# Performance work log

Hardware: AMD Instinct MI355X
Metric: run time of the kernel (lower is better)

The kernel has to match this reference:

```python
import jax, jax.numpy as jnp
import numpy as np

N = 12288
D = 128
NUM_BATCH = 32
EPS = 1e-8


def setup_inputs() -> dict:
    key = jax.random.key(0)
    kq, kk, kv, kb = jax.random.split(key, 4)
    Q = jax.random.normal(kq, (N, D), dtype=jnp.float32)
    K = jax.random.normal(kk, (N, D), dtype=jnp.float32)
    V = jax.random.normal(kv, (N, D), dtype=jnp.float32)
    batch_seg = jnp.sort(jax.random.randint(kb, (N,), 0, NUM_BATCH, dtype=jnp.int32))
    return {"Q": Q, "K": K, "V": V, "num_batch": NUM_BATCH, "batch_seg": batch_seg}


def reference(Q, K, V, num_batch, batch_seg):
    d = Q.shape[-1]
    dot = Q @ K.T                                   # [N, N]
    # NOTE: faithful to original: subtract GLOBAL max, then divide by sqrt(d)
    A = jnp.exp((dot - jnp.max(dot)) / jnp.sqrt(jnp.float32(d)))
    if num_batch > 1:
        mask = (batch_seg[None, :] == batch_seg[:, None])  # block-diagonal
        A = jnp.where(mask, A, jnp.zeros((), A.dtype))
    norm = jnp.sum(A, axis=-1, keepdims=True) + EPS
    A_weights = A / norm
    return A_weights @ V
```

## Files before the change

### kernel.cpp

```cpp
#include <hip/hip_runtime.h>


#define NN 12288
#define DD 128
#define NB 32
#define PS_LD 40
#define VTS 12424

typedef __attribute__((ext_vector_type(8))) short short8;
typedef __attribute__((ext_vector_type(4))) float float4v;

__device__ __forceinline__ short f2bf(float f) {
  unsigned u = __builtin_bit_cast(unsigned, f);
  return (short)((u + 0x7FFFu + ((u >> 16) & 1u)) >> 16);
}

__device__ __forceinline__ float bf2f(short s) {
  return __builtin_bit_cast(float, ((unsigned)(unsigned short)s) << 16);
}

__device__ __forceinline__ short8 ld8_bf16(const float* p) {
  float4v f0 = *(const float4v*)p;
  float4v f1 = *(const float4v*)(p + 4);
  short8 s;
  s[0] = f2bf(f0[0]); s[1] = f2bf(f0[1]); s[2] = f2bf(f0[2]); s[3] = f2bf(f0[3]);
  s[4] = f2bf(f1[0]); s[5] = f2bf(f1[1]); s[6] = f2bf(f1[2]); s[7] = f2bf(f1[3]);
  return s;
}

__device__ __forceinline__ void dma16(const short* gsrc, short* ldst) {
  auto g = (const __attribute__((address_space(1))) void*)(unsigned long long)gsrc;
  auto l = (__attribute__((address_space(3))) void*)(unsigned)(unsigned long long)ldst;
  __builtin_amdgcn_global_load_lds(g, l, 16, 0, 0);
}

__global__ __launch_bounds__(256) void prep_kernel(
    const float* __restrict__ K, const float* __restrict__ V,
    const int* __restrict__ seg,
    short* __restrict__ Kb, short* __restrict__ Vtb, int* __restrict__ starts) {
  const int tid = threadIdx.x;
  const int b = blockIdx.x;
  if (b < 768) {
    const size_t base = (size_t)b * 2048 + (size_t)tid * 8;
    *(short8*)(Kb + base) = ld8_bf16(K + base);
  } else if (b < 864) {
    __shared__ __align__(16) short Ts[DD * 136];
    const int kt = (b - 768) * 128;
#pragma unroll
    for (int rep = 0; rep < 16; ++rep) {
      int v = rep * 256 + tid;
      int key = v >> 5, c4 = (v & 31) * 4;
      float4v f = *(const float4v*)(V + (size_t)(kt + key) * DD + c4);
      Ts[(c4 + 0) * 136 + key] = f2bf(f[0]);
      Ts[(c4 + 1) * 136 + key] = f2bf(f[1]);
      Ts[(c4 + 2) * 136 + key] = f2bf(f[2]);
      Ts[(c4 + 3) * 136 + key] = f2bf(f[3]);
    }
    __syncthreads();
    const int c16 = (tid & 15) * 8;
#pragma unroll
    for (int rep = 0; rep < 8; ++rep) {
      int d = rep * 16 + (tid >> 4);
      short8 s = *(const short8*)&Ts[d * 136 + c16];
      *(short8*)(Vtb + (size_t)d * VTS + kt + c16) = s;
    }
  } else {
    int i = (b - 864) * 256 + tid;
    int s = seg[i];
    int sp = (i == 0) ? -1 : seg[i - 1];
    for (int bb = sp + 1; bb <= s; ++bb) starts[bb] = i;
    if (i == NN - 1)
      for (int bb = s + 1; bb <= NB; ++bb) starts[bb] = NN;
  }
}

__device__ __forceinline__ void issue_tile(
    const short* __restrict__ Kb, const short* __restrict__ Vtb,
    short* KshP, short* VshP, int j0, int wave, int lane) {
#pragma unroll
  for (int i = 0; i < 2; ++i) {
    const int R = wave * 8 + i * 4;
    const int row = R + (lane >> 4);
    const int dchunk = (lane & 15) ^ (row & 15);
    dma16(Kb + (size_t)(j0 + row) * DD + dchunk * 8, KshP + R * 128);
  }
#pragma unroll
  for (int i = 0; i < 2; ++i) {
    const int D = wave * 32 + i * 16;
    const int dr = D + (lane >> 2);
    const int vchunk = (lane & 3) ^ ((lane >> 2) & 3);
    dma16(Vtb + (size_t)dr * VTS + j0 + vchunk * 8, VshP + D * 32);
  }
}

__global__ __launch_bounds__(256, 4) void attn_kernel(
    const float* __restrict__ Q, const short* __restrict__ Kb,
    const short* __restrict__ Vtb, const int* __restrict__ seg,
    const int* __restrict__ starts,
    short* __restrict__ Op, float* __restrict__ lp) {
  __shared__ __align__(16) short Ksh[2][32 * 128];
  __shared__ __align__(16) short Vsh[2][128 * 32];
  __shared__ __align__(16) short Ps[4][16 * PS_LD];

  const int tid = threadIdx.x;
  const int wave = tid >> 6;
  const int lane = tid & 63;
  const int c = lane & 15;
  const int quad = lane >> 4;

  const int bid = blockIdx.x;
  const int y = bid >> 3;
  const int rg = (bid & 7) * 24 + (y >> 2);
  const int sk = y & 3;
  const int i0 = rg * 64;
  const int i0w = i0 + wave * 16;

  const int L = starts[seg[i0]];
  const int H = starts[seg[i0 + 63] + 1];
  const int Lm = L & ~31;
  const int nck = (H - Lm + 31) >> 5;
  const int ck0 = (nck * sk) >> 2;
  const int ck1 = (nck * (sk + 1)) >> 2;
  const int nt = ck1 - ck0;

  int st_r[4], en_r[4];
#pragma unroll
  for (int r = 0; r < 4; ++r) {
    int s = seg[i0w + quad * 4 + r];
    st_r[r] = starts[s];
    en_r[r] = starts[s + 1];
  }

  short8 qf[4];
  {
    const float* qrow = Q + (size_t)(i0w + c) * DD + quad * 8;
#pragma unroll
    for (int kc = 0; kc < 4; ++kc) qf[kc] = ld8_bf16(qrow + kc * 32);
  }

  float4v acc[8];
#pragma unroll
  for (int n = 0; n < 8; ++n) acc[n] = (float4v){0.f, 0.f, 0.f, 0.f};
  float l_part[4] = {0.f, 0.f, 0.f, 0.f};

  const float scale = 0.08838834764831845f;

  if (nt > 0)
    issue_tile(Kb, Vtb, &Ksh[0][0], &Vsh[0][0], Lm + ck0 * 32, wave, lane);
  __syncthreads();

  for (int t = 0; t < nt; ++t) {
    const int j0 = Lm + (ck0 + t) * 32;
    const int p = t & 1;
    if (t + 1 < nt)
      issue_tile(Kb, Vtb, &Ksh[p ^ 1][0], &Vsh[p ^ 1][0], j0 + 32, wave, lane);

    float4v s0 = (float4v){0.f, 0.f, 0.f, 0.f};
    float4v s1 = (float4v){0.f, 0.f, 0.f, 0.f};
    const short* Kp = &Ksh[p][0];
#pragma unroll
    for (int kc = 0; kc < 4; ++kc) {
      const int pos = ((kc * 4 + quad) ^ c) * 8;
      short8 b0 = *(const short8*)(Kp + c * 128 + pos);
      short8 b1 = *(const short8*)(Kp + (16 + c) * 128 + pos);
      s0 = __builtin_amdgcn_mfma_f32_16x16x32_bf16(qf[kc], b0, s0, 0, 0, 0);
      s1 = __builtin_amdgcn_mfma_f32_16x16x32_bf16(qf[kc], b1, s1, 0, 0, 0);
    }

    const int ja = j0 + c, jb = ja + 16;
    short* prow = &Ps[wave][0];
#pragma unroll
    for (int r = 0; r < 4; ++r) {
      float pa = (ja >= st_r[r] && ja < en_r[r]) ? __expf(s0[r] * scale) : 0.f;
      float pb = (jb >= st_r[r] && jb < en_r[r]) ? __expf(s1[r] * scale) : 0.f;
      l_part[r] += pa + pb;
      int row = quad * 4 + r;
      prow[row * PS_LD + c]      = f2bf(pa);
      prow[row * PS_LD + 16 + c] = f2bf(pb);
    }
    short8 pf = *(const short8*)&Ps[wave][c * PS_LD + quad * 8];

    const short* Vp = &Vsh[p][0];
    const int vpos = (quad ^ (c & 3)) * 8;
#pragma unroll
    for (int n = 0; n < 8; ++n) {
      short8 vf = *(const short8*)(Vp + (n * 16 + c) * 32 + vpos);
      acc[n] = __builtin_amdgcn_mfma_f32_16x16x32_bf16(pf, vf, acc[n], 0, 0, 0);
    }

    __syncthreads();
  }

  float lrow[4];
#pragma unroll
  for (int r = 0; r < 4; ++r) {
    float l = l_part[r];
    l += __shfl_xor(l, 1, 64);
    l += __shfl_xor(l, 2, 64);
    l += __shfl_xor(l, 4, 64);
    l += __shfl_xor(l, 8, 64);
    lrow[r] = l;
  }

  short* OpW = Op + ((size_t)sk * NN + i0w) * DD;
#pragma unroll
  for (int n = 0; n < 8; ++n)
#pragma unroll
    for (int r = 0; r < 4; ++r)
      OpW[(quad * 4 + r) * DD + n * 16 + c] = f2bf(acc[n][r]);
  if (c == 0) {
#pragma unroll
    for (int r = 0; r < 4; ++r) lp[sk * NN + i0w + quad * 4 + r] = lrow[r];
  }
}

__global__ __launch_bounds__(256) void combine_kernel(
    const short* __restrict__ Op, const float* __restrict__ lp,
    float* __restrict__ out) {
  const int u = blockIdx.x * 256 + threadIdx.x;
  const int row = u >> 4, c8 = (u & 15) * 8;
  float l = lp[row] + lp[NN + row] + lp[2 * NN + row] + lp[3 * NN + row];
  float o[8] = {0.f, 0.f, 0.f, 0.f, 0.f, 0.f, 0.f, 0.f};
#pragma unroll
  for (int s = 0; s < 4; ++s) {
    short8 t = *(const short8*)(Op + ((size_t)s * NN + row) * DD + c8);
#pragma unroll
    for (int j = 0; j < 8; ++j) o[j] += bf2f(t[j]);
  }
  const float inv = 1.f / (l + 1e-8f);
  float4v o0 = (float4v){o[0] * inv, o[1] * inv, o[2] * inv, o[3] * inv};
  float4v o1 = (float4v){o[4] * inv, o[5] * inv, o[6] * inv, o[7] * inv};
  *(float4v*)(out + (size_t)row * DD + c8)     = o0;
  *(float4v*)(out + (size_t)row * DD + c8 + 4) = o1;
}

#define KT_LD 136
#define VT_LD 40
typedef __attribute__((ext_vector_type(4))) short short4v;

__global__ __launch_bounds__(256) void attn_fallback(
    const float* __restrict__ Q, const float* __restrict__ K,
    const float* __restrict__ V, const int* __restrict__ seg,
    float* __restrict__ out) {
  __shared__ __align__(16) short Kt[32 * KT_LD];
  __shared__ __align__(16) short Vt[DD * VT_LD];
  __shared__ __align__(16) short Ps[4][16 * PS_LD];
  const int tid = threadIdx.x, wave = tid >> 6, lane = tid & 63;
  const int c = lane & 15, quad = lane >> 4;
  const int m0 = blockIdx.x * 64, i0 = m0 + wave * 16;
  const int segFirst = seg[m0], segLast = seg[m0 + 63];
  int lo = 0, hb = NN;
  while (lo < hb) { int mid = (lo + hb) >> 1; if (seg[mid] < segFirst) lo = mid + 1; else hb = mid; }
  int hi = lo, hb2 = NN;
  while (hi < hb2) { int mid = (hi + hb2) >> 1; if (seg[mid] <= segLast) hi = mid + 1; else hb2 = mid; }
  short8 qf[4];
  const float* qrow = Q + (size_t)(i0 + c) * DD + quad * 8;
#pragma unroll
  for (int kc = 0; kc < 4; ++kc) qf[kc] = ld8_bf16(qrow + kc * 32);
  int seg_r[4];
#pragma unroll
  for (int r = 0; r < 4; ++r) seg_r[r] = seg[i0 + quad * 4 + r];
  float4v acc[8];
#pragma unroll
  for (int n = 0; n < 8; ++n) acc[n] = (float4v){0.f, 0.f, 0.f, 0.f};
  float l_part[4] = {0.f, 0.f, 0.f, 0.f};
  const float scale = 0.08838834764831845f;
  for (int j0 = lo; j0 < hi; j0 += 32) {
    __syncthreads();
    {
      int row = tid >> 3, ch = tid & 7;
      int jj = j0 + row; if (jj > NN - 1) jj = NN - 1;
      const float* kp = K + (size_t)jj * DD + ch * 16;
      short* dst = &Kt[row * KT_LD + ch * 16];
#pragma unroll
      for (int q4 = 0; q4 < 4; ++q4) {
        float4v f = *(const float4v*)(kp + q4 * 4);
        short4v s;
        s[0] = f2bf(f[0]); s[1] = f2bf(f[1]); s[2] = f2bf(f[2]); s[3] = f2bf(f[3]);
        *(short4v*)(dst + q4 * 4) = s;
      }
    }
    {
      int d = tid & 127, jh = tid >> 7;
      float vv[16];
#pragma unroll
      for (int j = 0; j < 16; ++j) {
        int jj = j0 + jh * 16 + j; if (jj > NN - 1) jj = NN - 1;
        vv[j] = V[(size_t)jj * DD + d];
      }
      short8 a, b2;
#pragma unroll
      for (int j = 0; j < 8; ++j) { a[j] = f2bf(vv[j]); b2[j] = f2bf(vv[8 + j]); }
      *(short8*)&Vt[d * VT_LD + jh * 16] = a;
      *(short8*)&Vt[d * VT_LD + jh * 16 + 8] = b2;
    }
    __syncthreads();
    float4v s0 = (float4v){0.f, 0.f, 0.f, 0.f};
    float4v s1 = (float4v){0.f, 0.f, 0.f, 0.f};
    const short* krow0 = &Kt[c * KT_LD + quad * 8];
    const short* krow1 = &Kt[(16 + c) * KT_LD + quad * 8];
#pragma unroll
    for (int kc = 0; kc < 4; ++kc) {
      short8 b0 = *(const short8*)(krow0 + kc * 32);
      short8 b1 = *(const short8*)(krow1 + kc * 32);
      s0 = __builtin_amdgcn_mfma_f32_16x16x32_bf16(qf[kc], b0, s0, 0, 0, 0);
      s1 = __builtin_amdgcn_mfma_f32_16x16x32_bf16(qf[kc], b1, s1, 0, 0, 0);
    }
    int ja = j0 + c, jb = ja + 16;
    int sa = seg[ja < NN ? ja : NN - 1];
    int sb = seg[jb < NN ? jb : NN - 1];
    bool va = ja < hi, vb = jb < hi;
    short* prow = &Ps[wave][0];
#pragma unroll
    for (int r = 0; r < 4; ++r) {
      float pa = (va && sa == seg_r[r]) ? __expf(s0[r] * scale) : 0.f;
      float pb = (vb && sb == seg_r[r]) ? __expf(s1[r] * scale) : 0.f;
      l_part[r] += pa + pb;
      int row = quad * 4 + r;
      prow[row * PS_LD + c] = f2bf(pa);
      prow[row * PS_LD + 16 + c] = f2bf(pb);
    }
    short8 pf = *(const short8*)&Ps[wave][c * PS_LD + quad * 8];
#pragma unroll
    for (int n = 0; n < 8; ++n) {
      short8 vfr = *(const short8*)&Vt[(n * 16 + c) * VT_LD + quad * 8];
      acc[n] = __builtin_amdgcn_mfma_f32_16x16x32_bf16(pf, vfr, acc[n], 0, 0, 0);
    }
  }
  float linv[4];
#pragma unroll
  for (int r = 0; r < 4; ++r) {
    float l = l_part[r];
    l += __shfl_xor(l, 1, 64);
    l += __shfl_xor(l, 2, 64);
    l += __shfl_xor(l, 4, 64);
    l += __shfl_xor(l, 8, 64);
    linv[r] = 1.f / (l + 1e-8f);
  }
#pragma unroll
  for (int n = 0; n < 8; ++n)
#pragma unroll
    for (int r = 0; r < 4; ++r)
      out[(size_t)(i0 + quad * 4 + r) * DD + n * 16 + c] = acc[n][r] * linv[r];
}

extern "C" void kernel_launch(void* const* d_in, const int* in_sizes, int n_in,
                              void* d_out, int out_size, void* d_ws, size_t ws_size,
                              hipStream_t stream) {
  const float* Q = (const float*)d_in[0];
  const float* K = (const float*)d_in[1];
  const float* V = (const float*)d_in[2];
  const int* seg = (const int*)d_in[4];
  float* out = (float*)d_out;

  const size_t kb_bytes = (size_t)NN * DD * sizeof(short);
  const size_t vt_bytes = (size_t)DD * VTS * sizeof(short);
  const size_t st_bytes = 64 * sizeof(int);
  const size_t op_bytes = (size_t)4 * NN * DD * sizeof(short);
  const size_t lp_bytes = (size_t)4 * NN * sizeof(float);
  const size_t need = kb_bytes + vt_bytes + st_bytes + op_bytes + lp_bytes;

  if (ws_size >= need) {
    char* w = (char*)d_ws;
    short* Kb  = (short*)w;                     w += kb_bytes;
    short* Vtb = (short*)w;                     w += vt_bytes;
    int* starts = (int*)w;                      w += st_bytes;
    short* Op = (short*)w;                      w += op_bytes;
    float* lp = (float*)w;
    prep_kernel<<<864 + NN / 256, 256, 0, stream>>>(K, V, seg, Kb, Vtb, starts);
    attn_kernel<<<768, 256, 0, stream>>>(Q, Kb, Vtb, seg, starts, Op, lp);
    combine_kernel<<<768, 256, 0, stream>>>(Op, lp, out);
  } else {
    attn_fallback<<<NN / 64, 256, 0, stream>>>(Q, K, V, seg, out);
  }
}
```

Measured before the change: 95.59 us.

## Fuse split-K combine into attention kernel and pre-swizzle V into tile-blocked layout

Drops the separate combine kernel and the bf16 partial-output buffers. The attention kernel now uses 512-thread blocks in which two wave groups each handle half of the key range and merge their results through shared memory before normalizing and writing out. Only 192 blocks are launched, against 768 four-way split blocks before, so fewer CUs may be busy and load balance can suffer. The V transpose is also rewritten to emit a per-32-key tile-blocked, pre-swizzled layout that each tile loads as contiguous DMAs, and the V prep is merged into the K-conversion blocks.

```diff
diff --git a/kernel.cpp b/kernel.cpp
--- a/kernel.cpp
+++ b/kernel.cpp
@@ -5,7 +5,6 @@
 #define DD 128
 #define NB 32
 #define PS_LD 40
-#define VTS 12424
 
 typedef __attribute__((ext_vector_type(8))) short short8;
 typedef __attribute__((ext_vector_type(4))) float float4v;
@@ -37,35 +36,22 @@
 __global__ __launch_bounds__(256) void prep_kernel(
     const float* __restrict__ K, const float* __restrict__ V,
     const int* __restrict__ seg,
-    short* __restrict__ Kb, short* __restrict__ Vtb, int* __restrict__ starts) {
+    short* __restrict__ Kb, short* __restrict__ Vt, int* __restrict__ starts) {
   const int tid = threadIdx.x;
   const int b = blockIdx.x;
   if (b < 768) {
-    const size_t base = (size_t)b * 2048 + (size_t)tid * 8;
+    const int r0 = ((b & 7) * 96 + (b >> 3)) * 16;
+    const size_t base = (size_t)r0 * DD + (size_t)tid * 8;
     *(short8*)(Kb + base) = ld8_bf16(K + base);
-  } else if (b < 864) {
-    __shared__ __align__(16) short Ts[DD * 136];
-    const int kt = (b - 768) * 128;
-#pragma unroll
-    for (int rep = 0; rep < 16; ++rep) {
-      int v = rep * 256 + tid;
-      int key = v >> 5, c4 = (v & 31) * 4;
-      float4v f = *(const float4v*)(V + (size_t)(kt + key) * DD + c4);
-      Ts[(c4 + 0) * 136 + key] = f2bf(f[0]);
-      Ts[(c4 + 1) * 136 + key] = f2bf(f[1]);
-      Ts[(c4 + 2) * 136 + key] = f2bf(f[2]);
-      Ts[(c4 + 3) * 136 + key] = f2bf(f[3]);
-    }
-    __syncthreads();
-    const int c16 = (tid & 15) * 8;
-#pragma unroll
-    for (int rep = 0; rep < 8; ++rep) {
-      int d = rep * 16 + (tid >> 4);
-      short8 s = *(const short8*)&Ts[d * 136 + c16];
-      *(short8*)(Vtb + (size_t)d * VTS + kt + c16) = s;
-    }
+    const int d = tid & 127;
+    const int k0 = r0 + (tid >> 7) * 8;
+    short8 sv;
+#pragma unroll
+    for (int j = 0; j < 8; ++j) sv[j] = f2bf(V[(size_t)(k0 + j) * DD + d]);
+    const int m = (k0 & 31) >> 3;
+    *(short8*)(Vt + (size_t)(k0 >> 5) * 4096 + d * 32 + ((m ^ (d & 3)) * 8)) = sv;
   } else {
-    int i = (b - 864) * 256 + tid;
+    int i = (b - 768) * 256 + tid;
     int s = seg[i];
     int sp = (i == 0) ? -1 : seg[i - 1];
     for (int bb = sp + 1; bb <= s; ++bb) starts[bb] = i;
@@ -74,61 +60,59 @@
   }
 }
 
-__device__ __forceinline__ void issue_tile(
-    const short* __restrict__ Kb, const short* __restrict__ Vtb,
-    short* KshP, short* VshP, int j0, int wave, int lane) {
+__device__ __forceinline__ void issue_tile2(
+    const short* __restrict__ Kb, const short* __restrict__ Vt,
+    short* KshP, short* VshP, int j0, int wq, int lane) {
 #pragma unroll
   for (int i = 0; i < 2; ++i) {
-    const int R = wave * 8 + i * 4;
+    const int R = wq * 8 + i * 4;
     const int row = R + (lane >> 4);
     const int dchunk = (lane & 15) ^ (row & 15);
     dma16(Kb + (size_t)(j0 + row) * DD + dchunk * 8, KshP + R * 128);
   }
+  const size_t vbase = (size_t)(j0 >> 5) * 4096;
 #pragma unroll
   for (int i = 0; i < 2; ++i) {
-    const int D = wave * 32 + i * 16;
-    const int dr = D + (lane >> 2);
-    const int vchunk = (lane & 3) ^ ((lane >> 2) & 3);
-    dma16(Vtb + (size_t)dr * VTS + j0 + vchunk * 8, VshP + D * 32);
-  }
-}
-
-__global__ __launch_bounds__(256, 4) void attn_kernel(
+    const int off = (wq * 2 + i) * 512;
+    dma16(Vt + vbase + off + lane * 8, VshP + off);
+  }
+}
+
+__global__ __launch_bounds__(512, 2) void attn_fused(
     const float* __restrict__ Q, const short* __restrict__ Kb,
-    const short* __restrict__ Vtb, const int* __restrict__ seg,
-    const int* __restrict__ starts,
-    short* __restrict__ Op, float* __restrict__ lp) {
-  __shared__ __align__(16) short Ksh[2][32 * 128];
-  __shared__ __align__(16) short Vsh[2][128 * 32];
-  __shared__ __align__(16) short Ps[4][16 * PS_LD];
+    const short* __restrict__ Vt, const int* __restrict__ seg,
+    const int* __restrict__ starts, float* __restrict__ out) {
+  __shared__ __align__(16) short Ksh[2][2][32 * 128];
+  __shared__ __align__(16) short Vsh[2][2][128 * 32];
+  __shared__ __align__(16) short Ps[8][16 * PS_LD];
 
   const int tid = threadIdx.x;
-  const int wave = tid >> 6;
+  const int w = tid >> 6;
   const int lane = tid & 63;
+  const int s = w & 1;
+  const int r = w >> 1;
   const int c = lane & 15;
   const int quad = lane >> 4;
 
   const int bid = blockIdx.x;
-  const int y = bid >> 3;
-  const int rg = (bid & 7) * 24 + (y >> 2);
-  const int sk = y & 3;
+  const int rg = (bid & 7) * 24 + (bid >> 3);
   const int i0 = rg * 64;
-  const int i0w = i0 + wave * 16;
+  const int i0w = i0 + r * 16;
 
   const int L = starts[seg[i0]];
   const int H = starts[seg[i0 + 63] + 1];
   const int Lm = L & ~31;
   const int nck = (H - Lm + 31) >> 5;
-  const int ck0 = (nck * sk) >> 2;
-  const int ck1 = (nck * (sk + 1)) >> 2;
-  const int nt = ck1 - ck0;
+  const int ck0 = s ? (nck >> 1) : 0;
+  const int nt = s ? (nck - (nck >> 1)) : (nck >> 1);
+  const int ntmax = nck - (nck >> 1);
 
   int st_r[4], en_r[4];
 #pragma unroll
-  for (int r = 0; r < 4; ++r) {
-    int s = seg[i0w + quad * 4 + r];
-    st_r[r] = starts[s];
-    en_r[r] = starts[s + 1];
+  for (int rr = 0; rr < 4; ++rr) {
+    int sv = seg[i0w + quad * 4 + rr];
+    st_r[rr] = starts[sv];
+    en_r[rr] = starts[sv + 1];
   }
 
   short8 qf[4];
@@ -146,92 +130,85 @@
   const float scale = 0.08838834764831845f;
 
   if (nt > 0)
-    issue_tile(Kb, Vtb, &Ksh[0][0], &Vsh[0][0], Lm + ck0 * 32, wave, lane);
+    issue_tile2(Kb, Vt, &Ksh[s][0][0], &Vsh[s][0][0], Lm + ck0 * 32, r, lane);
   __syncthreads();
 
-  for (int t = 0; t < nt; ++t) {
+  for (int t = 0; t < ntmax; ++t) {
+    const int p = t & 1;
     const int j0 = Lm + (ck0 + t) * 32;
-    const int p = t & 1;
     if (t + 1 < nt)
-      issue_tile(Kb, Vtb, &Ksh[p ^ 1][0], &Vsh[p ^ 1][0], j0 + 32, wave, lane);
-
-    float4v s0 = (float4v){0.f, 0.f, 0.f, 0.f};
-    float4v s1 = (float4v){0.f, 0.f, 0.f, 0.f};
-    const short* Kp = &Ksh[p][0];
-#pragma unroll
-    for (int kc = 0; kc < 4; ++kc) {
-      const int pos = ((kc * 4 + quad) ^ c) * 8;
-      short8 b0 = *(const short8*)(Kp + c * 128 + pos);
-      short8 b1 = *(const short8*)(Kp + (16 + c) * 128 + pos);
-      s0 = __builtin_amdgcn_mfma_f32_16x16x32_bf16(qf[kc], b0, s0, 0, 0, 0);
-      s1 = __builtin_amdgcn_mfma_f32_16x16x32_bf16(qf[kc], b1, s1, 0, 0, 0);
-    }
-
-    const int ja = j0 + c, jb = ja + 16;
-    short* prow = &Ps[wave][0];
-#pragma unroll
-    for (int r = 0; r < 4; ++r) {
-      float pa = (ja >= st_r[r] && ja < en_r[r]) ? __expf(s0[r] * scale) : 0.f;
-      float pb = (jb >= st_r[r] && jb < en_r[r]) ? __expf(s1[r] * scale) : 0.f;
-      l_part[r] += pa + pb;
-      int row = quad * 4 + r;
-      prow[row * PS_LD + c]      = f2bf(pa);
-      prow[row * PS_LD + 16 + c] = f2bf(pb);
-    }
-    short8 pf = *(const short8*)&Ps[wave][c * PS_LD + quad * 8];
-
-    const short* Vp = &Vsh[p][0];
-    const int vpos = (quad ^ (c & 3)) * 8;
-#pragma unroll
-    for (int n = 0; n < 8; ++n) {
-      short8 vf = *(const short8*)(Vp + (n * 16 + c) * 32 + vpos);
-      acc[n] = __builtin_amdgcn_mfma_f32_16x16x32_bf16(pf, vf, acc[n], 0, 0, 0);
+      issue_tile2(Kb, Vt, &Ksh[s][p ^ 1][0], &Vsh[s][p ^ 1][0], j0 + 32, r, lane);
+
+    if (t < nt) {
+      float4v sa = (float4v){0.f, 0.f, 0.f, 0.f};
+      float4v sb = (float4v){0.f, 0.f, 0.f, 0.f};
+      const short* Kp = &Ksh[s][p][0];
+#pragma unroll
+      for (int kc = 0; kc < 4; ++kc) {
+        const int pos = ((kc * 4 + quad) ^ c) * 8;
+        short8 b0 = *(const short8*)(Kp + c * 128 + pos);
+        short8 b1 = *(const short8*)(Kp + (16 + c) * 128 + pos);
+        sa = __builtin_amdgcn_mfma_f32_16x16x32_bf16(qf[kc], b0, sa, 0, 0, 0);
+        sb = __builtin_amdgcn_mfma_f32_16x16x32_bf16(qf[kc], b1, sb, 0, 0, 0);
+      }
+
+      const int ja = j0 + c, jb = ja + 16;
+      short* prow = &Ps[w][0];
+#pragma unroll
+      for (int rr = 0; rr < 4; ++rr) {
+        float pa = (ja >= st_r[rr] && ja < en_r[rr]) ? __expf(sa[rr] * scale) : 0.f;
+        float pb = (jb >= st_r[rr] && jb < en_r[rr]) ? __expf(sb[rr] * scale) : 0.f;
+        l_part[rr] += pa + pb;
+        int row = quad * 4 + rr;
+        prow[row * PS_LD + c]      = f2bf(pa);
+        prow[row * PS_LD + 16 + c] = f2bf(pb);
+      }
+      short8 pf = *(const short8*)&Ps[w][c * PS_LD + quad * 8];
+
+      const short* Vp = &Vsh[s][p][0];
+      const int vpos = (quad ^ (c & 3)) * 8;
+#pragma unroll
+      for (int n = 0; n < 8; ++n) {
+        short8 vf = *(const short8*)(Vp + (n * 16 + c) * 32 + vpos);
+        acc[n] = __builtin_amdgcn_mfma_f32_16x16x32_bf16(pf, vf, acc[n], 0, 0, 0);
+      }
     }
 
     __syncthreads();
   }
 
-  float lrow[4];
-#pragma unroll
-  for (int r = 0; r < 4; ++r) {
-    float l = l_part[r];
-    l += __shfl_xor(l, 1, 64);
-    l += __shfl_xor(l, 2, 64);
-    l += __shfl_xor(l, 4, 64);
-    l += __shfl_xor(l, 8, 64);
-    lrow[r] = l;
-  }
-
-  short* OpW = Op + ((size_t)sk * NN + i0w) * DD;
-#pragma unroll
-  for (int n = 0; n < 8; ++n)
-#pragma unroll
-    for (int r = 0; r < 4; ++r)
-      OpW[(quad * 4 + r) * DD + n * 16 + c] = f2bf(acc[n][r]);
-  if (c == 0) {
-#pragma unroll
-    for (int r = 0; r < 4; ++r) lp[sk * NN + i0w + quad * 4 + r] = lrow[r];
-  }
-}
-
-__global__ __launch_bounds__(256) void combine_kernel(
-    const short* __restrict__ Op, const float* __restrict__ lp,
-    float* __restrict__ out) {
-  const int u = blockIdx.x * 256 + threadIdx.x;
-  const int row = u >> 4, c8 = (u & 15) * 8;
-  float l = lp[row] + lp[NN + row] + lp[2 * NN + row] + lp[3 * NN + row];
-  float o[8] = {0.f, 0.f, 0.f, 0.f, 0.f, 0.f, 0.f, 0.f};
-#pragma unroll
-  for (int s = 0; s < 4; ++s) {
-    short8 t = *(const short8*)(Op + ((size_t)s * NN + row) * DD + c8);
-#pragma unroll
-    for (int j = 0; j < 8; ++j) o[j] += bf2f(t[j]);
-  }
-  const float inv = 1.f / (l + 1e-8f);
-  float4v o0 = (float4v){o[0] * inv, o[1] * inv, o[2] * inv, o[3] * inv};
-  float4v o1 = (float4v){o[4] * inv, o[5] * inv, o[6] * inv, o[7] * inv};
-  *(float4v*)(out + (size_t)row * DD + c8)     = o0;
-  *(float4v*)(out + (size_t)row * DD + c8 + 4) = o1;
+  float* Mf = reinterpret_cast<float*>(&Ksh[0][0][0]);
+  float* Lf = reinterpret_cast<float*>(&Vsh[0][0][0]);
+  const int ml = r * 64 + lane;
+  if (s == 1) {
+#pragma unroll
+    for (int n = 0; n < 8; ++n)
+      *(float4v*)(Mf + n * 1024 + ml * 4) = acc[n];
+#pragma unroll
+    for (int rr = 0; rr < 4; ++rr) Lf[rr * 256 + ml] = l_part[rr];
+  }
+  __syncthreads();
+  if (s == 0) {
+#pragma unroll
+    for (int n = 0; n < 8; ++n)
+      acc[n] += *(const float4v*)(Mf + n * 1024 + ml * 4);
+
+    float inv_r[4];
+#pragma unroll
+    for (int rr = 0; rr < 4; ++rr) {
+      float l = l_part[rr] + Lf[rr * 256 + ml];
+      l += __shfl_xor(l, 1, 64);
+      l += __shfl_xor(l, 2, 64);
+      l += __shfl_xor(l, 4, 64);
+      l += __shfl_xor(l, 8, 64);
+      inv_r[rr] = 1.f / (l + 1e-8f);
+    }
+#pragma unroll
+    for (int n = 0; n < 8; ++n)
+#pragma unroll
+      for (int rr = 0; rr < 4; ++rr)
+        out[(size_t)(i0w + quad * 4 + rr) * DD + n * 16 + c] = acc[n][rr] * inv_r[rr];
+  }
 }
 
 #define KT_LD 136
@@ -243,7 +220,7 @@
     const float* __restrict__ V, const int* __restrict__ seg,
     float* __restrict__ out) {
   __shared__ __align__(16) short Kt[32 * KT_LD];
-  __shared__ __align__(16) short Vt[DD * VT_LD];
+  __shared__ __align__(16) short Vtl[DD * VT_LD];
   __shared__ __align__(16) short Ps[4][16 * PS_LD];
   const int tid = threadIdx.x, wave = tid >> 6, lane = tid & 63;
   const int c = lane & 15, quad = lane >> 4;
@@ -275,9 +252,9 @@
 #pragma unroll
       for (int q4 = 0; q4 < 4; ++q4) {
         float4v f = *(const float4v*)(kp + q4 * 4);
-        short4v s;
-        s[0] = f2bf(f[0]); s[1] = f2bf(f[1]); s[2] = f2bf(f[2]); s[3] = f2bf(f[3]);
-        *(short4v*)(dst + q4 * 4) = s;
+        short4v sx;
+        sx[0] = f2bf(f[0]); sx[1] = f2bf(f[1]); sx[2] = f2bf(f[2]); sx[3] = f2bf(f[3]);
+        *(short4v*)(dst + q4 * 4) = sx;
       }
     }
     {
@@ -291,30 +268,30 @@
       short8 a, b2;
 #pragma unroll
       for (int j = 0; j < 8; ++j) { a[j] = f2bf(vv[j]); b2[j] = f2bf(vv[8 + j]); }
-      *(short8*)&Vt[d * VT_LD + jh * 16] = a;
-      *(short8*)&Vt[d * VT_LD + jh * 16 + 8] = b2;
+      *(short8*)&Vtl[d * VT_LD + jh * 16] = a;
+      *(short8*)&Vtl[d * VT_LD + jh * 16 + 8] = b2;
     }
     __syncthreads();
-    float4v s0 = (float4v){0.f, 0.f, 0.f, 0.f};
-    float4v s1 = (float4v){0.f, 0.f, 0.f, 0.f};
+    float4v sa = (float4v){0.f, 0.f, 0.f, 0.f};
+    float4v sb = (float4v){0.f, 0.f, 0.f, 0.f};
     const short* krow0 = &Kt[c * KT_LD + quad * 8];
     const short* krow1 = &Kt[(16 + c) * KT_LD + quad * 8];
 #pragma unroll
     for (int kc = 0; kc < 4; ++kc) {
       short8 b0 = *(const short8*)(krow0 + kc * 32);
       short8 b1 = *(const short8*)(krow1 + kc * 32);
-      s0 = __builtin_amdgcn_mfma_f32_16x16x32_bf16(qf[kc], b0, s0, 0, 0, 0);
-      s1 = __builtin_amdgcn_mfma_f32_16x16x32_bf16(qf[kc], b1, s1, 0, 0, 0);
+      sa = __builtin_amdgcn_mfma_f32_16x16x32_bf16(qf[kc], b0, sa, 0, 0, 0);
+      sb = __builtin_amdgcn_mfma_f32_16x16x32_bf16(qf[kc], b1, sb, 0, 0, 0);
     }
     int ja = j0 + c, jb = ja + 16;
-    int sa = seg[ja < NN ? ja : NN - 1];
-    int sb = seg[jb < NN ? jb : NN - 1];
+    int sa2 = seg[ja < NN ? ja : NN - 1];
+    int sb2 = seg[jb < NN ? jb : NN - 1];
     bool va = ja < hi, vb = jb < hi;
     short* prow = &Ps[wave][0];
 #pragma unroll
     for (int r = 0; r < 4; ++r) {
-      float pa = (va && sa == seg_r[r]) ? __expf(s0[r] * scale) : 0.f;
-      float pb = (vb && sb == seg_r[r]) ? __expf(s1[r] * scale) : 0.f;
+      float pa = (va && sa2 == seg_r[r]) ? __expf(sa[r] * scale) : 0.f;
+      float pb = (vb && sb2 == seg_r[r]) ? __expf(sb[r] * scale) : 0.f;
       l_part[r] += pa + pb;
       int row = quad * 4 + r;
       prow[row * PS_LD + c] = f2bf(pa);
@@ -323,7 +300,7 @@
     short8 pf = *(const short8*)&Ps[wave][c * PS_LD + quad * 8];
 #pragma unroll
     for (int n = 0; n < 8; ++n) {
-      short8 vfr = *(const short8*)&Vt[(n * 16 + c) * VT_LD + quad * 8];
+      short8 vfr = *(const short8*)&Vtl[(n * 16 + c) * VT_LD + quad * 8];
       acc[n] = __builtin_amdgcn_mfma_f32_16x16x32_bf16(pf, vfr, acc[n], 0, 0, 0);
     }
   }
@@ -354,22 +331,17 @@
   float* out = (float*)d_out;
 
   const size_t kb_bytes = (size_t)NN * DD * sizeof(short);
-  const size_t vt_bytes = (size_t)DD * VTS * sizeof(short);
+  const size_t vt_bytes = (size_t)NN * DD * sizeof(short);
   const size_t st_bytes = 64 * sizeof(int);
-  const size_t op_bytes = (size_t)4 * NN * DD * sizeof(short);
-  const size_t lp_bytes = (size_t)4 * NN * sizeof(float);
-  const size_t need = kb_bytes + vt_bytes + st_bytes + op_bytes + lp_bytes;
+  const size_t need = kb_bytes + vt_bytes + st_bytes;
 
   if (ws_size >= need) {
     char* w = (char*)d_ws;
-    short* Kb  = (short*)w;                     w += kb_bytes;
-    short* Vtb = (short*)w;                     w += vt_bytes;
-    int* starts = (int*)w;                      w += st_bytes;
-    short* Op = (short*)w;                      w += op_bytes;
-    float* lp = (float*)w;
-    prep_kernel<<<864 + NN / 256, 256, 0, stream>>>(K, V, seg, Kb, Vtb, starts);
-    attn_kernel<<<768, 256, 0, stream>>>(Q, Kb, Vtb, seg, starts, Op, lp);
-    combine_kernel<<<768, 256, 0, stream>>>(Op, lp, out);
+    short* Kb = (short*)w;      w += kb_bytes;
+    short* Vt = (short*)w;      w += vt_bytes;
+    int* starts = (int*)w;
+    prep_kernel<<<768 + NN / 256, 256, 0, stream>>>(K, V, seg, Kb, Vt, starts);
+    attn_fused<<<192, 512, 0, stream>>>(Q, Kb, Vt, seg, starts, out);
   } else {
     attn_fallback<<<NN / 64, 256, 0, stream>>>(Q, K, V, seg, out);
   }
```

New measurement: 94.70 us. About the same (-0.9%).
